# Performance work log

Hardware: AMD Instinct MI355X
Metric: run time of the kernel (lower is better)

## Reference

```python
import jax, jax.numpy as jnp
import numpy as np

S = 3      # num_scales
CIN = 3    # in_channels (hardcoded by expand(...,3,...) in source)
COUT = 3   # out_channels (forced by final broadcast)
K = 3
PAD = 1


def setup_inputs() -> dict:
    key = jax.random.key(0)
    ks = jax.random.split(key, 8)
    B, H, W = 4, 384, 384
    x = jax.random.normal(ks[0], (B, CIN, H, W), jnp.float32)
    # params follow the torch inits: theta,sigma ~ U(0,pi); f0,theta0 = 1
    theta = jax.random.uniform(ks[1], (S, COUT, CIN), jnp.float32) * jnp.pi
    sigma = jax.random.uniform(ks[2], (S, COUT, CIN), jnp.float32) * jnp.pi
    f0 = jnp.ones((S, COUT, CIN), jnp.float32)
    theta0 = jnp.ones((S, COUT, CIN), jnp.float32)
    attn_w1 = jax.random.normal(ks[3], (64, CIN), jnp.float32) * 0.1     # 1x1 conv weight
    attn_b1 = jnp.zeros((64,), jnp.float32)
    attn_w2 = jax.random.normal(ks[4], (COUT * S, 64), jnp.float32) * 0.1
    attn_b2 = jnp.zeros((COUT * S,), jnp.float32)
    conv_w = jax.random.normal(ks[5], (COUT, CIN, K, K), jnp.float32) * 0.05
    mixing = jax.random.uniform(ks[6], (1,), jnp.float32)
    band = jax.random.uniform(ks[7], (COUT, CIN, 2), jnp.float32)        # freq_band_select ~ U(0,1)
    return dict(x=x, theta=theta, sigma=sigma, f0=f0, theta0=theta0,
                attn_w1=attn_w1, attn_b1=attn_b1, attn_w2=attn_w2, attn_b2=attn_b2,
                conv_w=conv_w, mixing=mixing, band=band)


def _log_gabor_bank(theta, sigma, f0, theta0, H, W):
    # vectorized over all scales: returns [S, Co, Cin, H, W] real filter bank
    yy, xx = jnp.meshgrid(jnp.linspace(-1.0, 1.0, H), jnp.linspace(-1.0, 1.0, W), indexing='ij')
    r = jnp.sqrt(xx * xx + yy * yy + 1e-6)          # [H,W]
    phi = jnp.arctan2(yy, xx)                        # [H,W]
    f0e = f0[..., None, None]                        # [S,Co,Cin,1,1]
    sig = sigma[..., None, None]
    th = theta[..., None, None]
    th0 = theta0[..., None, None]
    log_gabor = jnp.exp(-jnp.log(r - jnp.log(f0e)) ** 2 / (2.0 * jnp.log(sig) ** 2))
    angular = jnp.exp(-(phi - th) ** 2 / (2.0 * th0 ** 2))
    return log_gabor * angular


def _forward(x, theta, sigma, f0, theta0, attn_w1, attn_b1, attn_w2, attn_b2, conv_w, mixing, band):
    B, Cin, H, W = x.shape
    # torch.fft.fftshift with no dim shifts ALL axes (incl. batch/channel) -- replicate exactly
    x_freq_shift = jnp.fft.fftshift(jnp.fft.fft2(x))                 # [B,Cin,H,W] complex64

    filt = _log_gabor_bank(theta, sigma, f0, theta0, H, W)           # [S,Co,Cin,H,W]

    # attention net: 1x1 conv -> relu -> 1x1 conv -> softmax over channel dim
    mag = jnp.abs(x_freq_shift)
    h1 = jax.nn.relu(jnp.einsum('bchw,oc->bohw', mag, attn_w1) + attn_b1[None, :, None, None])
    logits = jnp.einsum('bchw,oc->bohw', h1, attn_w2) + attn_b2[None, :, None, None]
    attn = jax.nn.softmax(logits, axis=1).reshape(B, S, COUT, H, W)

    # attended[b,d,h,w] = sum_{s,co} attn[b,s,co,h,w] * xfreq[b,d,h,w] * filt[s,co,d,h,w]
    wgt = jnp.einsum('bschw,scdhw->bdhw', attn, filt)                # real [B,Cin,H,W]
    attended = (x_freq_shift * wgt).sum(axis=1)                      # [B,H,W] complex

    # per-(out,in)-channel square band mask, indices from height (as in source)
    start_idx = jnp.floor((band[..., 0] + 1.0) / 2.0 * H).astype(jnp.int32)   # [Co,Cin]
    end_idx = jnp.floor((band[..., 1] + 1.0) / 2.0 * H).astype(jnp.int32)
    ih = jnp.arange(H)
    rm = (ih[None, None, :] >= start_idx[..., None]) & (ih[None, None, :] < end_idx[..., None])
    iw = jnp.arange(W)
    cm = (iw[None, None, :] >= start_idx[..., None]) & (iw[None, None, :] < end_idx[..., None])
    mask = (rm[..., :, None] & cm[..., None, :]).astype(x.dtype)     # [Co,Cin,H,W]

    # broadcast quirk in source: [B,1,H,W] * [B,Co,1,Cin,H,W] -> [B,Co,B,Cin,H,W]
    six = mask[None, :, None, :, :, :] * attended[None, None, :, None, :, :]
    six = jnp.broadcast_to(six, (B, COUT, B, Cin, H, W))
    # torch ifftshift with no dim shifts ALL 6 axes; ifft2 transforms last two
    x_filtered = jnp.fft.ifft2(jnp.fft.ifftshift(six)).real          # [B,Co,B,Cin,H,W]

    x_spatial = jax.lax.conv_general_dilated(
        x, conv_w, window_strides=(1, 1), padding=[(PAD, PAD), (PAD, PAD)],
        dimension_numbers=('NCHW', 'OIHW', 'NCHW'))                  # [B,Co,H,W]

    mix = mixing[0]
    return mix * x_filtered + (1.0 - mix) * x_spatial[None, None]    # [B,Co,B,Cin,H,W]


def reference(x, theta, sigma, f0, theta0, attn_w1, attn_b1, attn_w2, attn_b2, conv_w, mixing, band):
    return _forward(x, theta, sigma, f0, theta0, attn_w1, attn_b1, attn_w2, attn_b2, conv_w, mixing, band)
```

## Files before the change

kernel.cpp:

```cpp
#include <hip/hip_runtime.h>
#include <math.h>

#define N384 384
#define NPIX 147456
#define LSTRIDE 385
#define LINES 8

__device__ __forceinline__ float2 cmul(float2 a, float2 b) {
    return make_float2(a.x*b.x - a.y*b.y, a.x*b.y + a.y*b.x);
}

template <int NT>
__device__ __forceinline__ void build_tw(float2* tw, int tid) {
    for (int k = tid; k < 384; k += NT) {
        float sn, cs;
        sincospif((float)k * (2.0f / 384.0f), &sn, &cs);
        tw[k] = make_float2(cs, sn);
    }
}

template <int SGNI>
__device__ float2* fft384x8(float2* b0, float2* b1, const float2* tw, int tid) {
    float2* src = b0;
    float2* dst = b1;
    const int line = tid >> 5;
    const int l32  = tid & 31;
    const float SG = (float)SGNI;
    const float s3 = SG * 0.86602540378443864676f;

    {
        float2* L = src + line * LSTRIDE;
        float2* D = dst + line * LSTRIDE;
#pragma unroll
        for (int q = 0; q < 2; ++q) {
            int i = l32 + 32 * q;
            float2 e0 = L[i],       e1 = L[i + 128], e2 = L[i + 256];
            float2 o0 = L[i + 64],  o1 = L[i + 192], o2 = L[i + 320];
            float t1x = e1.x + e2.x, t1y = e1.y + e2.y;
            float t2x = e1.x - e2.x, t2y = e1.y - e2.y;
            float2 E0 = make_float2(e0.x + t1x, e0.y + t1y);
            float mx = e0.x - 0.5f * t1x, my = e0.y - 0.5f * t1y;
            float ux = -s3 * t2y, uy = s3 * t2x;
            float2 E1 = make_float2(mx + ux, my + uy);
            float2 E2 = make_float2(mx - ux, my - uy);
            float s1x = o1.x + o2.x, s1y = o1.y + o2.y;
            float s2x = o1.x - o2.x, s2y = o1.y - o2.y;
            float2 O0 = make_float2(o0.x + s1x, o0.y + s1y);
            float nx = o0.x - 0.5f * s1x, ny = o0.y - 0.5f * s1y;
            float vx = -s3 * s2y, vy = s3 * s2x;
            float2 O1 = make_float2(nx + vx, ny + vy);
            float2 O2 = make_float2(nx - vx, ny - vy);
            float2 T1 = make_float2(0.5f * O1.x - s3 * O1.y, 0.5f * O1.y + s3 * O1.x);
            float2 T2 = make_float2(-0.5f * O2.x - s3 * O2.y, -0.5f * O2.y + s3 * O2.x);
            float2 y0 = make_float2(E0.x + O0.x, E0.y + O0.y);
            float2 y3 = make_float2(E0.x - O0.x, E0.y - O0.y);
            float2 y1 = make_float2(E1.x + T1.x, E1.y + T1.y);
            float2 y4 = make_float2(E1.x - T1.x, E1.y - T1.y);
            float2 y2 = make_float2(E2.x + T2.x, E2.y + T2.y);
            float2 y5 = make_float2(E2.x - T2.x, E2.y - T2.y);
            float2 c1 = tw[i], c2 = tw[2 * i], c3 = tw[3 * i], c4 = tw[4 * i], c5 = tw[5 * i];
            int o = 6 * i;
            D[o]     = y0;
            D[o + 1] = cmul(y1, make_float2(c1.x, SG * c1.y));
            D[o + 2] = cmul(y2, make_float2(c2.x, SG * c2.y));
            D[o + 3] = cmul(y3, make_float2(c3.x, SG * c3.y));
            D[o + 4] = cmul(y4, make_float2(c4.x, SG * c4.y));
            D[o + 5] = cmul(y5, make_float2(c5.x, SG * c5.y));
        }
    }
    __syncthreads();
    { float2* t = src; src = dst; dst = t; }

#pragma unroll
    for (int st = 0; st < 2; ++st) {
        const int s = (st == 0) ? 6 : 24;
        float2* L = src + line * LSTRIDE;
        float2* D = dst + line * LSTRIDE;
#pragma unroll
        for (int q = 0; q < 3; ++q) {
            int i = l32 + 32 * q;
            int k = i % s;
            int js = i - k;
            float2 A0 = L[i];
            float2 A1 = L[i + 96];
            float2 A2 = L[i + 192];
            float2 A3 = L[i + 288];
            float t0x = A0.x + A2.x, t0y = A0.y + A2.y;
            float t1x = A0.x - A2.x, t1y = A0.y - A2.y;
            float t2x = A1.x + A3.x, t2y = A1.y + A3.y;
            float t3x = A1.x - A3.x, t3y = A1.y - A3.y;
            float u3x = -SG * t3y,   u3y = SG * t3x;
            float2 y0 = make_float2(t0x + t2x, t0y + t2y);
            float2 y2 = make_float2(t0x - t2x, t0y - t2y);
            float2 y1 = make_float2(t1x + u3x, t1y + u3y);
            float2 y3 = make_float2(t1x - u3x, t1y - u3y);
            float2 c1 = tw[js], c2 = tw[2 * js], c3 = tw[3 * js];
            float2 w1 = make_float2(c1.x, SG * c1.y);
            float2 w2 = make_float2(c2.x, SG * c2.y);
            float2 w3 = make_float2(c3.x, SG * c3.y);
            int o = i + 3 * js;
            D[o]         = y0;
            D[o + s]     = cmul(y1, w1);
            D[o + 2 * s] = cmul(y2, w2);
            D[o + 3 * s] = cmul(y3, w3);
        }
        __syncthreads();
        { float2* t = src; src = dst; dst = t; }
    }

    {
        float2* L = src + line * LSTRIDE;
        float2* D = dst + line * LSTRIDE;
#pragma unroll
        for (int q = 0; q < 3; ++q) {
            int i = l32 + 32 * q;
            float2 A0 = L[i];
            float2 A1 = L[i + 96];
            float2 A2 = L[i + 192];
            float2 A3 = L[i + 288];
            float t0x = A0.x + A2.x, t0y = A0.y + A2.y;
            float t1x = A0.x - A2.x, t1y = A0.y - A2.y;
            float t2x = A1.x + A3.x, t2y = A1.y + A3.y;
            float t3x = A1.x - A3.x, t3y = A1.y - A3.y;
            float u3x = -SG * t3y,   u3y = SG * t3x;
            D[i]       = make_float2(t0x + t2x, t0y + t2y);
            D[i + 96]  = make_float2(t1x + u3x, t1y + u3y);
            D[i + 192] = make_float2(t0x - t2x, t0y - t2y);
            D[i + 288] = make_float2(t1x - u3x, t1y - u3y);
        }
    }
    __syncthreads();
    return dst;
}

__global__ __launch_bounds__(256) void k_fwd_rows(const float* __restrict__ x,
                                                  float2* __restrict__ F1) {
    __shared__ float2 sbuf[2][LINES * LSTRIDE];
    __shared__ float2 tw[384];
    int img = blockIdx.y;
    int rg  = blockIdx.x;
    int tid = threadIdx.x;
    build_tw<256>(tw, tid);
    const float4* xim = (const float4*)(x + (size_t)img * NPIX + (size_t)rg * 16 * 384);
    for (int idx4 = tid; idx4 < 1536; idx4 += 256) {
        int row = idx4 / 96;
        int e   = (idx4 - row * 96) * 4;
        float4 v = xim[idx4];
        float* L = (float*)(sbuf[0] + (row >> 1) * LSTRIDE + e) + (row & 1);
        L[0] = v.x; L[2] = v.y; L[4] = v.z; L[6] = v.w;
    }
    __syncthreads();
    float2* res = fft384x8<-1>(sbuf[0], sbuf[1], tw, tid);
    float2* F1b = F1 + (size_t)img * NPIX + (size_t)rg * 16 * 384;
    for (int it = tid; it < 1536; it += 256) {
        int line = it / 192;
        int k2   = it - line * 192;
        const float2* L = res + line * LSTRIDE;
        float2 A = L[k2];
        int m = (k2 == 0) ? 0 : 384 - k2;
        float2 B = L[m];
        float2 X1 = make_float2(0.5f * (A.x + B.x), 0.5f * (A.y - B.y));
        float2 X2 = make_float2(0.5f * (A.y + B.y), 0.5f * (B.x - A.x));
        F1b[(size_t)(2 * line) * 384 + k2]     = X1;
        F1b[(size_t)(2 * line + 1) * 384 + k2] = X2;
    }
}

__global__ __launch_bounds__(256) void k_fwd_cols(const float2* __restrict__ In,
                                                  float2* __restrict__ Out) {
    __shared__ float2 sbuf[2][LINES * LSTRIDE];
    __shared__ float2 tw[384];
    int img = blockIdx.y;
    int cg  = blockIdx.x;
    int tid = threadIdx.x;
    build_tw<256>(tw, tid);
    const float4* inim = (const float4*)(In + (size_t)img * NPIX + cg * 8);
    int c = tid & 3, hb = tid >> 2;
    for (int q = 0; q < 6; ++q) {
        int h = hb + 64 * q;
        float4 v = inim[(size_t)h * 192 + c];
        sbuf[0][(2 * c) * LSTRIDE + h]     = make_float2(v.x, v.y);
        sbuf[0][(2 * c + 1) * LSTRIDE + h] = make_float2(v.z, v.w);
    }
    __syncthreads();
    float2* res = fft384x8<-1>(sbuf[0], sbuf[1], tw, tid);
    float4* outim = (float4*)(Out + (size_t)img * NPIX + cg * 8);
    for (int q = 0; q < 3; ++q) {
        int h = hb + 64 * q;
        float2 a = res[(2 * c) * LSTRIDE + h];
        float2 b = res[(2 * c + 1) * LSTRIDE + h];
        outim[(size_t)h * 192 + c] = make_float4(a.x, a.y, b.x, b.y);
    }
}

__global__ __launch_bounds__(192) void k_attn(const float2* __restrict__ F2,
                                              const float* __restrict__ theta,
                                              const float* __restrict__ sigma,
                                              const float* __restrict__ f0,
                                              const float* __restrict__ theta0,
                                              const float* __restrict__ aw1,
                                              const float* __restrict__ ab1,
                                              const float* __restrict__ aw2,
                                              const float* __restrict__ ab2,
                                              const float* __restrict__ band,
                                              float2* __restrict__ A) {
    __shared__ float4 par[27];
    int tid = threadIdx.x;
    if (tid < 27) {
        float lf0 = logf(f0[tid]);
        float ls  = logf(sigma[tid]);
        float na  = -0.5f / (ls * ls);
        float th  = theta[tid];
        float t0  = theta0[tid];
        float nb  = -0.5f / (t0 * t0);
        par[tid] = make_float4(lf0, na, th, nb);
    }
    __syncthreads();

    int h = 192 + blockIdx.x;
    int w = 192 + tid;

    bool needed = false;
#pragma unroll
    for (int q = 0; q < 9; ++q) {
        int s = (int)floorf((band[2 * q + 0] + 1.0f) * 0.5f * 384.0f);
        int e = (int)floorf((band[2 * q + 1] + 1.0f) * 0.5f * 384.0f);
        needed |= (h >= s) && (h < e) && (w >= s) && (w < e);
    }
    if (__ballot(needed) == 0ULL) return;

    int hs = h - 192;
    int ws = w - 192;

    float2 xf[4][3];
    float  mag[4][3];
#pragma unroll
    for (int b = 0; b < 4; ++b) {
        int bp = (b + 2) & 3;
#pragma unroll
        for (int c = 0; c < 3; ++c) {
            int cp = c + 2; if (cp >= 3) cp -= 3;
            float2 v = F2[(size_t)(bp * 3 + cp) * NPIX + (size_t)hs * 384 + ws];
            xf[b][c]  = v;
            mag[b][c] = sqrtf(v.x * v.x + v.y * v.y);
        }
    }

    float lgt[4][9];
#pragma unroll
    for (int b = 0; b < 4; ++b)
#pragma unroll
        for (int j = 0; j < 9; ++j) lgt[b][j] = ab2[j];
    for (int o = 0; o < 64; ++o) {
        float w0 = aw1[o * 3 + 0], w1 = aw1[o * 3 + 1], w2 = aw1[o * 3 + 2];
        float bb = ab1[o];
        float hv[4];
#pragma unroll
        for (int b = 0; b < 4; ++b)
            hv[b] = fmaxf(bb + w0 * mag[b][0] + w1 * mag[b][1] + w2 * mag[b][2], 0.0f);
#pragma unroll
        for (int j = 0; j < 9; ++j) {
            float wj = aw2[j * 64 + o];
#pragma unroll
            for (int b = 0; b < 4; ++b) lgt[b][j] += wj * hv[b];
        }
    }

    float yy = -1.0f + 2.0f * (float)h / 383.0f;
    float xx = -1.0f + 2.0f * (float)w / 383.0f;
    float r   = sqrtf(xx * xx + yy * yy + 1e-6f);
    float phi = atan2f(yy, xx);
    float filt[27];
#pragma unroll
    for (int i = 0; i < 27; ++i) {
        float4 pr = par[i];
        float lr = logf(r - pr.x);
        float dphi = phi - pr.z;
        filt[i] = expf(lr * lr * pr.y + dphi * dphi * pr.w);
    }

#pragma unroll
    for (int b = 0; b < 4; ++b) {
        float mxv = lgt[b][0];
#pragma unroll
        for (int j = 1; j < 9; ++j) mxv = fmaxf(mxv, lgt[b][j]);
        float e[9];
        float se = 0.0f;
#pragma unroll
        for (int j = 0; j < 9; ++j) { e[j] = expf(lgt[b][j] - mxv); se += e[j]; }
        float inv = 1.0f / se;

        float2 acc = make_float2(0.0f, 0.0f);
#pragma unroll
        for (int d = 0; d < 3; ++d) {
            float wg = 0.0f;
#pragma unroll
            for (int s = 0; s < 3; ++s)
#pragma unroll
                for (int co = 0; co < 3; ++co)
                    wg += e[s * 3 + co] * filt[(s * 3 + co) * 3 + d];
            wg *= inv;
            acc.x += xf[b][d].x * wg;
            acc.y += xf[b][d].y * wg;
        }
        if (needed)
            A[(size_t)b * NPIX + (size_t)h * 384 + w] = acc;
    }
}

__global__ __launch_bounds__(256) void k_masked_rows(const float2* __restrict__ A,
                                                     const float* __restrict__ band,
                                                     float2* __restrict__ G1c) {
    int ii  = blockIdx.y;
    int rg  = blockIdx.x;
    int cop = ii / 12;
    int bp  = (ii / 3) % 4;
    int dp  = ii % 3;
    int pidx = (cop * 3 + dp) * 2;
    int sidx = (int)floorf((band[pidx + 0] + 1.0f) * 0.5f * 384.0f);
    int eidx = (int)floorf((band[pidx + 1] + 1.0f) * 0.5f * 384.0f);
    if (eidx <= sidx) return;
    int h0 = 192 + rg * 8;
    if (h0 + 8 <= sidx || h0 >= eidx) return;

    __shared__ float2 sbuf[2][LINES * LSTRIDE];
    __shared__ float2 tw[384];
    int tid = threadIdx.x;
    build_tw<256>(tw, tid);
    const float2* Ab = A + (size_t)bp * NPIX;
    for (int idx = tid; idx < 8 * 384; idx += 256) {
        int line = idx / 384;
        int w    = idx - line * 384;
        int h    = h0 + line;
        bool m = (h >= sidx) && (h < eidx) && (w >= sidx) && (w < eidx);
        float2 v = make_float2(0.0f, 0.0f);
        if (m) v = Ab[(size_t)h * 384 + w];
        sbuf[0][line * LSTRIDE + w] = v;
    }
    __syncthreads();
    float2* res = fft384x8<1>(sbuf[0], sbuf[1], tw, tid);
    for (int idx = tid; idx < 8 * 384; idx += 256) {
        int line = idx / 384;
        int w    = idx - line * 384;
        int h    = h0 + line;
        if (h >= sidx && h < eidx) {
            float2 v = res[line * LSTRIDE + w];
            if (w & 1) { v.x = -v.x; v.y = -v.y; }
            G1c[((size_t)ii * 192 + (h - sidx)) * 384 + w] = v;
        }
    }
}

__global__ __launch_bounds__(128) void k_col_gemm_combine(const float2* __restrict__ G1c,
                                                          const float* __restrict__ band,
                                                          const float* __restrict__ x,
                                                          const float* __restrict__ cw,
                                                          const float* __restrict__ mixing,
                                                          float* __restrict__ out) {
    __shared__ float2 tw[384];
    int tid = threadIdx.x;
    build_tw<128>(tw, tid);

    int ii  = blockIdx.y;
    int gt  = blockIdx.x * 128 + tid;
    int wq  = gt % 96;
    int hg  = gt / 96;
    int w   = wq * 4;
    int h0  = hg * 8;

    int cop = ii / 12;
    int bp  = (ii / 3) % 4;
    int dp  = ii % 3;
    int pidx = (cop * 3 + dp) * 2;
    int sidx = (int)floorf((band[pidx + 0] + 1.0f) * 0.5f * 384.0f);
    int eidx = (int)floorf((band[pidx + 1] + 1.0f) * 0.5f * 384.0f);
    __syncthreads();

    float acc[8][4];
#pragma unroll
    for (int r = 0; r < 8; ++r)
#pragma unroll
        for (int j = 0; j < 4; ++j) acc[r][j] = 0.0f;

    if (eidx > sidx) {
        float2 t[8], rot[8];
#pragma unroll
        for (int r = 0; r < 8; ++r) {
            int h = h0 + r;
            t[r]   = tw[(sidx * h) % 384];
            rot[r] = tw[h];
        }
        const float4* g = (const float4*)(G1c + (size_t)ii * 192 * 384 + w);
        for (int hp = sidx; hp < eidx; ++hp) {
            float4 g0 = g[(size_t)(hp - sidx) * 192];
            float4 g1 = g[(size_t)(hp - sidx) * 192 + 1];
#pragma unroll
            for (int r = 0; r < 8; ++r) {
                float tx = t[r].x, ty = t[r].y;
                acc[r][0] += tx * g0.x - ty * g0.y;
                acc[r][1] += tx * g0.z - ty * g0.w;
                acc[r][2] += tx * g1.x - ty * g1.y;
                acc[r][3] += tx * g1.z - ty * g1.w;
                t[r] = make_float2(tx * rot[r].x - ty * rot[r].y,
                                   tx * rot[r].y + ty * rot[r].x);
            }
        }
    }

    int co = cop + 2; if (co >= 3) co -= 3;
    int b  = (bp + 2) & 3;
    int d  = dp + 2;  if (d >= 3) d -= 3;

    float wv[3][9];
#pragma unroll
    for (int ci = 0; ci < 3; ++ci)
#pragma unroll
        for (int t9 = 0; t9 < 9; ++t9) wv[ci][t9] = cw[((size_t)d * 3 + ci) * 9 + t9];

    float cacc[8][4];
#pragma unroll
    for (int r = 0; r < 8; ++r)
#pragma unroll
        for (int j = 0; j < 4; ++j) cacc[r][j] = 0.0f;
    const float* xb = x + (size_t)b * 3 * NPIX;
#pragma unroll
    for (int ci = 0; ci < 3; ++ci) {
        const float* xc = xb + (size_t)ci * NPIX;
#pragma unroll
        for (int ihh = 0; ihh < 10; ++ihh) {
            int hh = h0 - 1 + ihh;
            if (hh < 0 || hh >= 384) continue;
            const float* xr = xc + (size_t)hh * 384;
            float v[6];
#pragma unroll
            for (int c6 = 0; c6 < 6; ++c6) {
                int ww = w - 1 + c6;
                v[c6] = (ww >= 0 && ww < 384) ? xr[ww] : 0.0f;
            }
#pragma unroll
            for (int r = 0; r < 8; ++r) {
                int kr = ihh - r;
                if (kr < 0 || kr > 2) continue;
#pragma unroll
                for (int j = 0; j < 4; ++j)
#pragma unroll
                    for (int kw = 0; kw < 3; ++kw)
                        cacc[r][j] += v[j + kw] * wv[ci][kr * 3 + kw];
            }
        }
    }

    float mix  = mixing[0];
    float omix = 1.0f - mix;
    const float invn2 = 1.0f / 147456.0f;
    float* obase = out + (size_t)(co * 12 + b * 3 + d) * NPIX;
#pragma unroll
    for (int r = 0; r < 8; ++r) {
        int h = h0 + r;
        float sgn = (h & 1) ? -invn2 : invn2;
        size_t off = (size_t)h * 384 + w;
        float4 val;
        val.x = mix * (acc[r][0] * sgn) + omix * cacc[r][0];
        val.y = mix * (acc[r][1] * sgn) + omix * cacc[r][1];
        val.z = mix * (acc[r][2] * sgn) + omix * cacc[r][2];
        val.w = mix * (acc[r][3] * sgn) + omix * cacc[r][3];
#pragma unroll
        for (int a = 0; a < 4; ++a)
            *(float4*)(obase + off + (size_t)a * 5308416) = val;
    }
}

extern "C" void kernel_launch(void* const* d_in, const int* in_sizes, int n_in,
                              void* d_out, int out_size, void* d_ws, size_t ws_size,
                              hipStream_t stream) {
    const float* x      = (const float*)d_in[0];
    const float* theta  = (const float*)d_in[1];
    const float* sigma  = (const float*)d_in[2];
    const float* f0     = (const float*)d_in[3];
    const float* theta0 = (const float*)d_in[4];
    const float* aw1    = (const float*)d_in[5];
    const float* ab1    = (const float*)d_in[6];
    const float* aw2    = (const float*)d_in[7];
    const float* ab2    = (const float*)d_in[8];
    const float* cw     = (const float*)d_in[9];
    const float* mixing = (const float*)d_in[10];
    const float* band   = (const float*)d_in[11];
    float* out = (float*)d_out;

    float2* F1  = (float2*)d_ws;
    float2* F2  = F1 + (size_t)12 * NPIX;
    float2* G1c = (float2*)d_ws;
    float2* A   = (float2*)d_ws + (size_t)36 * NPIX;

    k_fwd_rows<<<dim3(24, 12), 256, 0, stream>>>(x, F1);
    k_fwd_cols<<<dim3(24, 12), 256, 0, stream>>>(F1, F2);
    k_attn<<<192, 192, 0, stream>>>(F2, theta, sigma, f0, theta0,
                                    aw1, ab1, aw2, ab2, band, A);
    k_masked_rows<<<dim3(24, 36), 256, 0, stream>>>(A, band, G1c);
    k_col_gemm_combine<<<dim3(36, 36), 128, 0, stream>>>(G1c, band, x, cw, mixing, out);
}
```

Measured before the change: 204.7 us.

## Split column DFT reduction across wavefront halves and reduce with cross-lane shuffle

Each 8x4 output tile is now handled by two lanes, 32 apart in a wavefront, instead of one. Each lane sums half of the masked frequency range, the partials are combined with a shfl_xor by 32, and each lane then writes 4 of the 8 rows, including its own share of the spatial conv. The grid doubles so there are twice as many threads working on the serial reduction loop, which shortens the per-thread critical path and raises occupancy. The cost is the shuffle and select step, plus the twiddle start computed per half.

```diff
diff --git a/kernel.cpp b/kernel.cpp
--- a/kernel.cpp
+++ b/kernel.cpp
@@ -361,12 +361,17 @@
     int tid = threadIdx.x;
     build_tw<128>(tw, tid);
 
-    int ii  = blockIdx.y;
-    int gt  = blockIdx.x * 128 + tid;
-    int wq  = gt % 96;
-    int hg  = gt / 96;
-    int w   = wq * 4;
-    int h0  = hg * 8;
+    int lane = tid & 63;
+    int wv   = tid >> 6;
+    int l32  = lane & 31;
+    int half = lane >> 5;
+
+    int ii   = blockIdx.y;
+    int tile = blockIdx.x * 64 + wv * 32 + l32;
+    int wq   = tile % 96;
+    int hg   = tile / 96;
+    int w    = wq * 4;
+    int h0   = hg * 8;
 
     int cop = ii / 12;
     int bp  = (ii / 3) % 4;
@@ -382,16 +387,21 @@
 #pragma unroll
         for (int j = 0; j < 4; ++j) acc[r][j] = 0.0f;
 
-    if (eidx > sidx) {
+    int L = eidx - sidx;
+    if (L > 0) {
+        int chunk = (L + 1) >> 1;
+        int myS = sidx + half * chunk;
+        int myE = myS + chunk; if (myE > eidx) myE = eidx;
+
         float2 t[8], rot[8];
 #pragma unroll
         for (int r = 0; r < 8; ++r) {
             int h = h0 + r;
-            t[r]   = tw[(sidx * h) % 384];
+            t[r]   = tw[(myS * h) % 384];
             rot[r] = tw[h];
         }
         const float4* g = (const float4*)(G1c + (size_t)ii * 192 * 384 + w);
-        for (int hp = sidx; hp < eidx; ++hp) {
+        for (int hp = myS; hp < myE; ++hp) {
             float4 g0 = g[(size_t)(hp - sidx) * 192];
             float4 g1 = g[(size_t)(hp - sidx) * 192 + 1];
 #pragma unroll
@@ -407,19 +417,33 @@
         }
     }
 
+#pragma unroll
+    for (int r = 0; r < 8; ++r)
+#pragma unroll
+        for (int j = 0; j < 4; ++j)
+            acc[r][j] += __shfl_xor(acc[r][j], 32);
+
+    float accs[4][4];
+#pragma unroll
+    for (int r = 0; r < 4; ++r)
+#pragma unroll
+        for (int j = 0; j < 4; ++j)
+            accs[r][j] = half ? acc[r + 4][j] : acc[r][j];
+    int hc = h0 + 4 * half;
+
     int co = cop + 2; if (co >= 3) co -= 3;
     int b  = (bp + 2) & 3;
     int d  = dp + 2;  if (d >= 3) d -= 3;
 
-    float wv[3][9];
+    float wv9[3][9];
 #pragma unroll
     for (int ci = 0; ci < 3; ++ci)
 #pragma unroll
-        for (int t9 = 0; t9 < 9; ++t9) wv[ci][t9] = cw[((size_t)d * 3 + ci) * 9 + t9];
-
-    float cacc[8][4];
-#pragma unroll
-    for (int r = 0; r < 8; ++r)
+        for (int t9 = 0; t9 < 9; ++t9) wv9[ci][t9] = cw[((size_t)d * 3 + ci) * 9 + t9];
+
+    float cacc[4][4];
+#pragma unroll
+    for (int r = 0; r < 4; ++r)
 #pragma unroll
         for (int j = 0; j < 4; ++j) cacc[r][j] = 0.0f;
     const float* xb = x + (size_t)b * 3 * NPIX;
@@ -427,8 +451,8 @@
     for (int ci = 0; ci < 3; ++ci) {
         const float* xc = xb + (size_t)ci * NPIX;
 #pragma unroll
-        for (int ihh = 0; ihh < 10; ++ihh) {
-            int hh = h0 - 1 + ihh;
+        for (int ihh = 0; ihh < 6; ++ihh) {
+            int hh = hc - 1 + ihh;
             if (hh < 0 || hh >= 384) continue;
             const float* xr = xc + (size_t)hh * 384;
             float v[6];
@@ -438,14 +462,14 @@
                 v[c6] = (ww >= 0 && ww < 384) ? xr[ww] : 0.0f;
             }
 #pragma unroll
-            for (int r = 0; r < 8; ++r) {
+            for (int r = 0; r < 4; ++r) {
                 int kr = ihh - r;
                 if (kr < 0 || kr > 2) continue;
 #pragma unroll
                 for (int j = 0; j < 4; ++j)
 #pragma unroll
                     for (int kw = 0; kw < 3; ++kw)
-                        cacc[r][j] += v[j + kw] * wv[ci][kr * 3 + kw];
+                        cacc[r][j] += v[j + kw] * wv9[ci][kr * 3 + kw];
             }
         }
     }
@@ -455,15 +479,15 @@
     const float invn2 = 1.0f / 147456.0f;
     float* obase = out + (size_t)(co * 12 + b * 3 + d) * NPIX;
 #pragma unroll
-    for (int r = 0; r < 8; ++r) {
-        int h = h0 + r;
+    for (int r = 0; r < 4; ++r) {
+        int h = hc + r;
         float sgn = (h & 1) ? -invn2 : invn2;
         size_t off = (size_t)h * 384 + w;
         float4 val;
-        val.x = mix * (acc[r][0] * sgn) + omix * cacc[r][0];
-        val.y = mix * (acc[r][1] * sgn) + omix * cacc[r][1];
-        val.z = mix * (acc[r][2] * sgn) + omix * cacc[r][2];
-        val.w = mix * (acc[r][3] * sgn) + omix * cacc[r][3];
+        val.x = mix * (accs[r][0] * sgn) + omix * cacc[r][0];
+        val.y = mix * (accs[r][1] * sgn) + omix * cacc[r][1];
+        val.z = mix * (accs[r][2] * sgn) + omix * cacc[r][2];
+        val.w = mix * (accs[r][3] * sgn) + omix * cacc[r][3];
 #pragma unroll
         for (int a = 0; a < 4; ++a)
             *(float4*)(obase + off + (size_t)a * 5308416) = val;
@@ -497,5 +521,5 @@
     k_attn<<<192, 192, 0, stream>>>(F2, theta, sigma, f0, theta0,
                                     aw1, ab1, aw2, ab2, band, A);
     k_masked_rows<<<dim3(24, 36), 256, 0, stream>>>(A, band, G1c);
-    k_col_gemm_combine<<<dim3(36, 36), 128, 0, stream>>>(G1c, band, x, cw, mixing, out);
-}
+    k_col_gemm_combine<<<dim3(72, 36), 128, 0, stream>>>(G1c, band, x, cw, mixing, out);
+}
```

New measurement: 217.8 us. 6.4% more time.
